# Kernel tuning notes

Measured on AMD Instinct MI355X. Metric: run time of the kernel, lower is better.

Reference implementation:

```python
import jax, jax.numpy as jnp
import numpy as np

DIM = 256
NUM_HEADS = 8
HEAD_DIM = DIM // NUM_HEADS  # 32
SCALE = HEAD_DIM ** (-0.5)


def _conv1x1(x, w, b):
    # x: [B,C,H,W], w: [O,C,1,1], b: [O]
    return jnp.einsum('bchw,oc->bohw', x, w[:, :, 0, 0]) + b[None, :, None, None]


def _dwconv3x3(x, w, b):
    # depthwise conv, groups=C, padding=1 (SAME)
    y = jax.lax.conv_general_dilated(
        x, w, window_strides=(1, 1), padding='SAME',
        feature_group_count=x.shape[1],
        dimension_numbers=('NCHW', 'OIHW', 'NCHW'))
    return y + b[None, :, None, None]


def setup_inputs() -> dict:
    key = jax.random.key(0)
    ks = jax.random.split(key, 9)
    s = 0.05
    return {
        'x': jax.random.normal(ks[0], (4, DIM, 48, 48), jnp.float32),
        'w_qk': jax.random.normal(ks[1], (2 * DIM, DIM, 1, 1), jnp.float32) * s,
        'b_qk': jax.random.normal(ks[2], (2 * DIM,), jnp.float32) * s,
        'w_v': jax.random.normal(ks[3], (DIM, DIM, 1, 1), jnp.float32) * s,
        'b_v': jax.random.normal(ks[4], (DIM,), jnp.float32) * s,
        'w_pe': jax.random.normal(ks[5], (DIM, 1, 3, 3), jnp.float32) * s,
        'b_pe': jax.random.normal(ks[6], (DIM,), jnp.float32) * s,
        'w_proj': jax.random.normal(ks[7], (DIM, DIM, 1, 1), jnp.float32) * s,
        'b_proj': jax.random.normal(ks[8], (DIM,), jnp.float32) * s,
    }


def reference(x, w_qk, b_qk, w_v, b_v, w_pe, b_pe, w_proj, b_proj):
    B, C, H, W = x.shape
    N = H * W
    h, d = NUM_HEADS, HEAD_DIM

    qk = _conv1x1(x, w_qk, b_qk).reshape(B, h, 2 * d, N)
    v4 = _conv1x1(x, w_v, b_v)                # [B,C,H,W]
    pe = _dwconv3x3(v4, w_pe, b_pe)           # [B,C,H,W]
    v = v4.reshape(B, h, d, N)

    q, k = qk[:, :, :d, :], qk[:, :, d:, :]   # [B,h,d,N] each
    attn = jnp.einsum('bhdi,bhdj->bhij', q, k) * SCALE  # [B,h,N,N]
    attn = jax.nn.softmax(attn, axis=-1)
    out = jnp.einsum('bhdj,bhij->bhdi', v, attn)        # [B,h,d,N]
    out = out.reshape(B, C, H, W)

    return _conv1x1(out + pe, w_proj, b_proj)
```

## Files before the change

kernel.cpp:

```cpp
#include <hip/hip_runtime.h>
#include <hip/hip_bf16.h>

#define NPIX 2304
#define HW 48
#define CDIM 256
#define NHEADS 8
#define HD 32
#define SCALE_CONST 0.17677669529663687f
#define LOG2E 1.4426950408889634f

typedef __attribute__((ext_vector_type(8))) short  short8v;
typedef __attribute__((ext_vector_type(4))) short  short4v;
typedef __attribute__((ext_vector_type(4))) float  floatx4;

__device__ inline short f2bf(float f) {
    unsigned u = __builtin_bit_cast(unsigned, f);
    u += 0x7FFFu + ((u >> 16) & 1u);
    return (short)(u >> 16);
}
__device__ inline float bf2f(unsigned short us) {
    return __builtin_bit_cast(float, (unsigned)us << 16);
}
__device__ inline float fexp2(float x) {
    return __builtin_amdgcn_exp2f(x);
}

__global__ __launch_bounds__(256) void prep_kernel(
    const float* __restrict__ x,
    short* __restrict__ XT,
    const float* __restrict__ wqk, const float* __restrict__ wv,
    const float* __restrict__ wp,
    short* __restrict__ wqkb, short* __restrict__ wvb, short* __restrict__ wpb)
{
    const int bx = blockIdx.x;
    const int t = threadIdx.x;
    if (bx >= 576) {
        int tid = (bx - 576) * 256 + t;
        for (int idx = tid; idx < 262144; idx += 16384) {
            if (idx < 131072)       wqkb[idx] = f2bf(wqk[idx]);
            else if (idx < 196608)  wvb[idx - 131072] = f2bf(wv[idx - 131072]);
            else                    wpb[idx - 196608] = f2bf(wp[idx - 196608]);
        }
        return;
    }
    __shared__ float sT[64][65];
    const int nt = bx % 36, ct = (bx / 36) & 3, b = bx / 144;
    const int c0 = ct * 64, n0 = nt * 64;
    const float* sp = x + ((size_t)b * 256 + c0) * NPIX + n0;
    const int cl = t >> 6, n = t & 63;
#pragma unroll
    for (int it = 0; it < 16; ++it) {
        int c = it * 4 + cl;
        sT[n][c] = sp[(size_t)c * NPIX + n];
    }
    __syncthreads();
    const int nr = t >> 2, q = t & 3;
    short out[16];
#pragma unroll
    for (int j = 0; j < 16; ++j) out[j] = f2bf(sT[nr][q * 16 + j]);
    short* dp = XT + ((size_t)b * NPIX + n0 + nr) * 256 + c0 + q * 16;
    *(int4*)dp = *(int4*)out;
    *(int4*)(dp + 8) = *(int4*)(out + 8);
}

#define XROW 528

__device__ inline void stage_xt_tile(const short* __restrict__ src_base,
                                     char* __restrict__ sX, int t)
{
    const short* src = src_base + (size_t)(t >> 3) * 256 + (t & 7) * 32;
    char* dst = sX + (t >> 3) * XROW + (t & 7) * 64;
#pragma unroll
    for (int rr = 0; rr < 2; ++rr) {
        const short* s = src + rr * 32 * 256;
        char* d = dst + rr * 32 * XROW;
        *(int4*)d        = *(const int4*)s;
        *(int4*)(d + 16) = *(const int4*)(s + 8);
        *(int4*)(d + 32) = *(const int4*)(s + 16);
        *(int4*)(d + 48) = *(const int4*)(s + 24);
    }
}

__global__ __launch_bounds__(256) void conv_qkv_mfma(
    const short* __restrict__ Wqk,
    const short* __restrict__ Wv,
    const float* __restrict__ bqk,
    const float* __restrict__ bv,
    const short* __restrict__ XT,
    short* __restrict__ QT,
    short* __restrict__ KT,
    short* __restrict__ VB)
{
    __shared__ __align__(16) char sX[64 * XROW];
    const int n0 = blockIdx.x * 64;
    const int b  = blockIdx.z;
    const int t = threadIdx.x, lane = t & 63, w = t >> 6;
    const int l15 = lane & 15, quad = lane >> 4;

    stage_xt_tile(XT + ((size_t)b * NPIX + n0) * 256, sX, t);
    __syncthreads();

    floatx4 accs[2][4];
#pragma unroll
    for (int g = 0; g < 2; ++g) {
        const int og = blockIdx.y + g * 6;
        const bool isV = (og >= 8);
        const short* Wb = isV ? Wv + (size_t)((og - 8) * 64 + w * 16 + l15) * CDIM
                              : Wqk + (size_t)(og * 64 + w * 16 + l15) * CDIM;
#pragma unroll
        for (int ib = 0; ib < 4; ++ib) accs[g][ib] = (floatx4){0.f, 0.f, 0.f, 0.f};
#pragma unroll
        for (int s = 0; s < 8; ++s) {
            short8v af = *(const short8v*)(Wb + s * 32 + quad * 8);
#pragma unroll
            for (int ib = 0; ib < 4; ++ib) {
                short8v bf = *(const short8v*)(sX + (ib * 16 + l15) * XROW + s * 64 + quad * 16);
                accs[g][ib] = __builtin_amdgcn_mfma_f32_16x16x32_bf16(af, bf, accs[g][ib], 0, 0, 0);
            }
        }
    }

#pragma unroll
    for (int g = 0; g < 2; ++g) {
        const int og = blockIdx.y + g * 6;
        const bool isV = (og >= 8);
        __syncthreads();
        if (!isV) {
            const bool isQ = (w < 2);
            const float scl = isQ ? SCALE_CONST * LOG2E : 1.0f;
            float bvv[4];
#pragma unroll
            for (int r = 0; r < 4; ++r) bvv[r] = bqk[og * 64 + w * 16 + quad * 4 + r];
#pragma unroll
            for (int ib = 0; ib < 4; ++ib) {
                short pb[4];
#pragma unroll
                for (int r = 0; r < 4; ++r) pb[r] = f2bf((accs[g][ib][r] + bvv[r]) * scl);
                *(short4v*)(sX + (ib * 16 + l15) * 136 + (w * 16 + quad * 4) * 2) = *(short4v*)pb;
            }
            __syncthreads();
            const int n = t >> 2, q = t & 3;
            int4 v0 = *(const int4*)(sX + n * 136 + q * 32);
            int4 v1 = *(const int4*)(sX + n * 136 + q * 32 + 16);
            short* dst = ((q < 2) ? QT : KT)
                       + ((size_t)(b * 8 + og) * NPIX + n0 + n) * HD + (q & 1) * 16;
            *(int4*)dst = v0;
            *(int4*)(dst + 8) = v1;
        } else {
            const int o0 = (og - 8) * 64 + w * 16 + quad * 4;
            float bvv[4];
#pragma unroll
            for (int r = 0; r < 4; ++r) bvv[r] = bv[o0 + r];
#pragma unroll
            for (int ib = 0; ib < 4; ++ib) {
                short pb[4];
#pragma unroll
                for (int r = 0; r < 4; ++r) pb[r] = f2bf(accs[g][ib][r] + bvv[r]);
                *(short4v*)(sX + (ib * 16 + l15) * 132 + (w * 16 + quad * 4) * 2) = *(short4v*)pb;
            }
            __syncthreads();
            const int o = t >> 2, q = t & 3;
            short tmp[16];
#pragma unroll
            for (int k = 0; k < 16; ++k)
                tmp[k] = *(const short*)(sX + (q * 16 + k) * 132 + o * 2);
            short* dst = VB + ((size_t)b * 256 + (og - 8) * 64 + o) * NPIX + n0 + q * 16;
            *(int4*)dst = *(int4*)tmp;
            *(int4*)(dst + 8) = *(int4*)(tmp + 8);
        }
    }
}

#define DROW 170

__global__ __launch_bounds__(256) void dwconv3x3_t(
    const short* __restrict__ VB,
    const float* __restrict__ Wp,
    const float* __restrict__ bp,
    short* __restrict__ PEt)
{
    __shared__ short spl[32 * DROW];
    const int n0 = blockIdx.x * 64;
    const int c0 = blockIdx.y * 32;
    const int b  = blockIdx.z;
    const int t  = threadIdx.x;

    for (int ch8 = t; ch8 < 672; ch8 += 256) {
        int ch = ch8 / 21, off = (ch8 % 21) * 8;
        int base = n0 - 52 + off;
        const short* src = VB + ((size_t)b * 256 + c0 + ch) * NPIX;
        short tmp[8];
        if (base >= 0 && base + 8 <= NPIX) {
            *(int4*)tmp = *(const int4*)(src + base);
        } else {
#pragma unroll
            for (int u = 0; u < 8; ++u) {
                int p = base + u;
                tmp[u] = (p >= 0 && p < NPIX) ? src[p] : (short)0;
            }
        }
        *(int4*)&spl[ch * DROW + off] = *(int4*)tmp;
    }
    __syncthreads();

    const int cl = t & 31;
    const int g8 = t >> 5;
    const int c  = c0 + cl;
    float wv[9];
#pragma unroll
    for (int k = 0; k < 9; ++k) wv[k] = Wp[c * 9 + k];
    const float bb = bp[c];

    const int px0  = n0 + g8 * 8;
    const int col0 = px0 % HW;
    const short* sprow = &spl[cl * DROW + 52 + g8 * 8];

#pragma unroll
    for (int u = 0; u < 8; ++u) {
        int colu = col0 + u; if (colu >= HW) colu -= HW;
        const bool okL = (colu != 0), okR = (colu != HW - 1);
        float a = bb;
#pragma unroll
        for (int dy = 0; dy < 3; ++dy) {
            int ci = u + (dy - 1) * HW;
            float m = bf2f((unsigned short)sprow[ci]);
            a += wv[dy * 3 + 1] * m;
            if (okL) a += wv[dy * 3 + 0] * bf2f((unsigned short)sprow[ci - 1]);
            if (okR) a += wv[dy * 3 + 2] * bf2f((unsigned short)sprow[ci + 1]);
        }
        PEt[((size_t)b * NPIX + px0 + u) * 256 + c] = f2bf(a);
    }
}

#define KROW 72
#define VROW 136
#define PROW 136
#define SK0 0
#define SK1 4608
#define SV0 9216
#define SV1 13568
#define SP0 17920
#define FL_SMEM 26624

__global__ __launch_bounds__(256) void flash_attn_mfma(
    const short* __restrict__ QT,
    const short* __restrict__ KT,
    const short* __restrict__ VB,
    const short* __restrict__ PEt,
    short* __restrict__ ST)
{
    __shared__ __align__(16) char smem[FL_SMEM];

    const int i0 = blockIdx.x * 64;
    const int bh = blockIdx.y;
    const int b  = bh >> 3, hh = bh & 7;

    const short* KTp = KT + (size_t)bh * NPIX * HD;
    const short* Vp  = VB + (size_t)(b * 256 + hh * HD) * NPIX;

    const int t    = threadIdx.x;
    const int lane = t & 63;
    const int w    = t >> 6;
    const int l15  = lane & 15;
    const int quad = lane >> 4;

    const short8v qfrag = *(const short8v*)(
        QT + ((size_t)bh * NPIX + i0 + w * 16 + l15) * HD + quad * 8);

    short8v ones;
#pragma unroll
    for (int k = 0; k < 8; ++k) ones[k] = (short)0x3F80;

    char* const sPw = smem + SP0 + w * (16 * PROW);

    floatx4 oacc[2], lacc;
    oacc[0] = (floatx4){0.f, 0.f, 0.f, 0.f};
    oacc[1] = (floatx4){0.f, 0.f, 0.f, 0.f};
    lacc    = (floatx4){0.f, 0.f, 0.f, 0.f};

    const short* ksrc = KTp + (size_t)(t >> 2) * HD + (t & 3) * 8;
    const short* vsrc = Vp + (size_t)(t >> 3) * NPIX + (t & 7) * 8;
    const int koff = (t >> 2) * KROW + (t & 3) * 16;
    const int voff = (t >> 3) * VROW + (t & 7) * 16;

    int4 kst = *(const int4*)ksrc;
    int4 vst = *(const int4*)vsrc;

    for (int it = 0; it < 36; ++it) {
        char* bufK = smem + ((it & 1) ? SK1 : SK0);
        char* bufV = smem + ((it & 1) ? SV1 : SV0);
        *(int2*)(bufK + koff)     = *(int2*)&kst;
        *(int2*)(bufK + koff + 8) = *((int2*)&kst + 1);
        *(int2*)(bufV + voff)     = *(int2*)&vst;
        *(int2*)(bufV + voff + 8) = *((int2*)&vst + 1);
        if (it + 1 < 36) {
            kst = *(const int4*)(ksrc + (size_t)(it + 1) * 64 * HD);
            vst = *(const int4*)(vsrc + (it + 1) * 64);
        }
        __syncthreads();

        floatx4 sacc[4];
#pragma unroll
        for (int jb = 0; jb < 4; ++jb) {
            const char* ka = bufK + (jb * 16 + l15) * KROW + quad * 16;
            short8v af;
            ((int2*)&af)[0] = *(const int2*)ka;
            ((int2*)&af)[1] = *(const int2*)(ka + 8);
            sacc[jb] = __builtin_amdgcn_mfma_f32_16x16x32_bf16(
                af, qfrag, (floatx4){0.f, 0.f, 0.f, 0.f}, 0, 0, 0);
        }

#pragma unroll
        for (int jb = 0; jb < 4; ++jb) {
            unsigned tb[4];
#pragma unroll
            for (int r = 0; r < 4; ++r)
                tb[r] = __builtin_bit_cast(unsigned, fexp2(sacc[jb][r]));
            int2 pw;
            pw.x = (int)__builtin_amdgcn_perm(tb[1], tb[0], 0x07060302u);
            pw.y = (int)__builtin_amdgcn_perm(tb[3], tb[2], 0x07060302u);
            *(int2*)(sPw + l15 * PROW + jb * 32 + quad * 8) = pw;
        }

#pragma unroll
        for (int ks = 0; ks < 2; ++ks) {
            const char* pa = sPw + l15 * PROW + ks * 64 + quad * 16;
            short8v pf;
            ((int2*)&pf)[0] = *(const int2*)pa;
            ((int2*)&pf)[1] = *(const int2*)(pa + 8);
#pragma unroll
            for (int db = 0; db < 2; ++db) {
                const char* va = bufV + (db * 16 + l15) * VROW + ks * 64 + quad * 16;
                short8v vf;
                ((int2*)&vf)[0] = *(const int2*)va;
                ((int2*)&vf)[1] = *(const int2*)(va + 8);
                oacc[db] = __builtin_amdgcn_mfma_f32_16x16x32_bf16(vf, pf, oacc[db], 0, 0, 0);
            }
            lacc = __builtin_amdgcn_mfma_f32_16x16x32_bf16(ones, pf, lacc, 0, 0, 0);
        }
    }

    const float invl = 1.0f / lacc[0];
    const int i = i0 + w * 16 + l15;
    const short* pep = PEt + ((size_t)b * NPIX + i) * 256 + hh * HD;
    short* stp = ST + ((size_t)b * NPIX + i) * 256 + hh * HD;
#pragma unroll
    for (int db = 0; db < 2; ++db) {
        short4v pev = *(const short4v*)(pep + db * 16 + quad * 4);
        short pb[4];
#pragma unroll
        for (int r = 0; r < 4; ++r) {
            float v = oacc[db][r] * invl + bf2f((unsigned short)pev[r]);
            pb[r] = f2bf(v);
        }
        *(short4v*)(stp + db * 16 + quad * 4) = *(short4v*)pb;
    }
}

__global__ __launch_bounds__(256) void conv_proj_mfma(
    const short* __restrict__ Wb,
    const float* __restrict__ bias,
    const short* __restrict__ ST,
    float* __restrict__ out)
{
    __shared__ __align__(16) char sX[64 * XROW];
    const int n0 = blockIdx.x * 64;
    const int og = blockIdx.y;
    const int b  = blockIdx.z;
    const int t = threadIdx.x, lane = t & 63, w = t >> 6;
    const int l15 = lane & 15, quad = lane >> 4;

    stage_xt_tile(ST + ((size_t)b * NPIX + n0) * 256, sX, t);
    __syncthreads();

    const short* Arow = Wb + (size_t)(og * 64 + w * 16 + l15) * CDIM;
    floatx4 acc[4];
#pragma unroll
    for (int ib = 0; ib < 4; ++ib) acc[ib] = (floatx4){0.f, 0.f, 0.f, 0.f};
#pragma unroll
    for (int s = 0; s < 8; ++s) {
        short8v af = *(const short8v*)(Arow + s * 32 + quad * 8);
#pragma unroll
        for (int ib = 0; ib < 4; ++ib) {
            short8v bf = *(const short8v*)(sX + (ib * 16 + l15) * XROW + s * 64 + quad * 16);
            acc[ib] = __builtin_amdgcn_mfma_f32_16x16x32_bf16(af, bf, acc[ib], 0, 0, 0);
        }
    }
    __syncthreads();

    {
        float bvv[4];
#pragma unroll
        for (int r = 0; r < 4; ++r) bvv[r] = bias[og * 64 + w * 16 + quad * 4 + r];
        float* sRep = (float*)sX;
#pragma unroll
        for (int r = 0; r < 4; ++r)
#pragma unroll
            for (int ib = 0; ib < 4; ++ib)
                sRep[(w * 16 + quad * 4 + r) * 68 + ib * 16 + l15] = acc[ib][r] + bvv[r];
    }
    __syncthreads();

    const int o = t >> 2, q = t & 3;
    const float* src = (const float*)sX + o * 68 + q * 16;
    float* dst = out + ((size_t)b * 256 + og * 64 + o) * NPIX + n0 + q * 16;
#pragma unroll
    for (int k = 0; k < 4; ++k)
        *(int4*)(dst + k * 4) = *(const int4*)(src + k * 4);
}

extern "C" void kernel_launch(void* const* d_in, const int* in_sizes, int n_in,
                              void* d_out, int out_size, void* d_ws, size_t ws_size,
                              hipStream_t stream) {
    const float* x      = (const float*)d_in[0];
    const float* w_qk   = (const float*)d_in[1];
    const float* b_qk   = (const float*)d_in[2];
    const float* w_v    = (const float*)d_in[3];
    const float* b_v    = (const float*)d_in[4];
    const float* w_pe   = (const float*)d_in[5];
    const float* b_pe   = (const float*)d_in[6];
    const float* w_proj = (const float*)d_in[7];
    const float* b_proj = (const float*)d_in[8];
    float* out = (float*)d_out;

    char* wsb = (char*)d_ws;
    short* ws_xt  = (short*)wsb;  wsb += (size_t)4 * NPIX * 256 * 2;
    short* ws_qt  = (short*)wsb;  wsb += (size_t)32 * NPIX * HD * 2;
    short* ws_kt  = (short*)wsb;  wsb += (size_t)32 * NPIX * HD * 2;
    short* ws_vb  = (short*)wsb;  wsb += (size_t)4 * 256 * NPIX * 2;
    short* ws_pet = (short*)wsb;  wsb += (size_t)4 * NPIX * 256 * 2;
    short* ws_st  = (short*)wsb;  wsb += (size_t)4 * NPIX * 256 * 2;
    short* ws_wqk = (short*)wsb;  wsb += (size_t)512 * 256 * 2;
    short* ws_wv  = (short*)wsb;  wsb += (size_t)256 * 256 * 2;
    short* ws_wp  = (short*)wsb;  wsb += (size_t)256 * 256 * 2;

    prep_kernel<<<dim3(640), 256, 0, stream>>>(x, ws_xt, w_qk, w_v, w_proj,
                                               ws_wqk, ws_wv, ws_wp);
    conv_qkv_mfma<<<dim3(36, 6, 4), 256, 0, stream>>>(ws_wqk, ws_wv, b_qk, b_v,
                                                      ws_xt, ws_qt, ws_kt, ws_vb);
    dwconv3x3_t<<<dim3(36, 8, 4), 256, 0, stream>>>(ws_vb, w_pe, b_pe, ws_pet);
    flash_attn_mfma<<<dim3(36, 32), 256, 0, stream>>>(ws_qt, ws_kt, ws_vb, ws_pet, ws_st);
    conv_proj_mfma<<<dim3(36, 4, 4), 256, 0, stream>>>(ws_wp, b_proj, ws_st, out);
}
```

Before: 161.0 us.

## Fuse depthwise 3x3 positional conv into output projection kernel

Removes the standalone depthwise-conv kernel and its PE intermediate buffer. The projection kernel now stages V halos for all 256 channels, computes the 3x3 depthwise conv itself, adds the result to the staged attention output tile in shared memory, and then runs the projection GEMM. Each block now covers two output-channel groups, so the grid halves. This saves one launch plus a write and read of the PE tensor. In exchange, every projection block recomputes the dwconv for all channels, which means redundant work across the 2 y-blocks, and the larger shared-memory footprint may lower occupancy.

New measurement: 179.3 us. 1.11x slower.

```diff
diff --git a/kernel.cpp b/kernel.cpp
--- a/kernel.cpp
+++ b/kernel.cpp
@@ -171,67 +171,6 @@
     }
 }
 
-#define DROW 170
-
-__global__ __launch_bounds__(256) void dwconv3x3_t(
-    const short* __restrict__ VB,
-    const float* __restrict__ Wp,
-    const float* __restrict__ bp,
-    short* __restrict__ PEt)
-{
-    __shared__ short spl[32 * DROW];
-    const int n0 = blockIdx.x * 64;
-    const int c0 = blockIdx.y * 32;
-    const int b  = blockIdx.z;
-    const int t  = threadIdx.x;
-
-    for (int ch8 = t; ch8 < 672; ch8 += 256) {
-        int ch = ch8 / 21, off = (ch8 % 21) * 8;
-        int base = n0 - 52 + off;
-        const short* src = VB + ((size_t)b * 256 + c0 + ch) * NPIX;
-        short tmp[8];
-        if (base >= 0 && base + 8 <= NPIX) {
-            *(int4*)tmp = *(const int4*)(src + base);
-        } else {
-#pragma unroll
-            for (int u = 0; u < 8; ++u) {
-                int p = base + u;
-                tmp[u] = (p >= 0 && p < NPIX) ? src[p] : (short)0;
-            }
-        }
-        *(int4*)&spl[ch * DROW + off] = *(int4*)tmp;
-    }
-    __syncthreads();
-
-    const int cl = t & 31;
-    const int g8 = t >> 5;
-    const int c  = c0 + cl;
-    float wv[9];
-#pragma unroll
-    for (int k = 0; k < 9; ++k) wv[k] = Wp[c * 9 + k];
-    const float bb = bp[c];
-
-    const int px0  = n0 + g8 * 8;
-    const int col0 = px0 % HW;
-    const short* sprow = &spl[cl * DROW + 52 + g8 * 8];
-
-#pragma unroll
-    for (int u = 0; u < 8; ++u) {
-        int colu = col0 + u; if (colu >= HW) colu -= HW;
-        const bool okL = (colu != 0), okR = (colu != HW - 1);
-        float a = bb;
-#pragma unroll
-        for (int dy = 0; dy < 3; ++dy) {
-            int ci = u + (dy - 1) * HW;
-            float m = bf2f((unsigned short)sprow[ci]);
-            a += wv[dy * 3 + 1] * m;
-            if (okL) a += wv[dy * 3 + 0] * bf2f((unsigned short)sprow[ci - 1]);
-            if (okR) a += wv[dy * 3 + 2] * bf2f((unsigned short)sprow[ci + 1]);
-        }
-        PEt[((size_t)b * NPIX + px0 + u) * 256 + c] = f2bf(a);
-    }
-}
-
 #define KROW 72
 #define VROW 136
 #define PROW 136
@@ -246,7 +185,6 @@
     const short* __restrict__ QT,
     const short* __restrict__ KT,
     const short* __restrict__ VB,
-    const short* __restrict__ PEt,
     short* __restrict__ ST)
 {
     __shared__ __align__(16) char smem[FL_SMEM];
@@ -342,71 +280,138 @@
 
     const float invl = 1.0f / lacc[0];
     const int i = i0 + w * 16 + l15;
-    const short* pep = PEt + ((size_t)b * NPIX + i) * 256 + hh * HD;
     short* stp = ST + ((size_t)b * NPIX + i) * 256 + hh * HD;
 #pragma unroll
     for (int db = 0; db < 2; ++db) {
-        short4v pev = *(const short4v*)(pep + db * 16 + quad * 4);
         short pb[4];
 #pragma unroll
-        for (int r = 0; r < 4; ++r) {
-            float v = oacc[db][r] * invl + bf2f((unsigned short)pev[r]);
-            pb[r] = f2bf(v);
-        }
+        for (int r = 0; r < 4; ++r)
+            pb[r] = f2bf(oacc[db][r] * invl);
         *(short4v*)(stp + db * 16 + quad * 4) = *(short4v*)pb;
     }
 }
 
-__global__ __launch_bounds__(256) void conv_proj_mfma(
+#define DROW 170
+#define PD_SMEM (64 * XROW + 64 * DROW * 2)
+
+__global__ __launch_bounds__(256) void conv_proj_dw_mfma(
     const short* __restrict__ Wb,
     const float* __restrict__ bias,
+    const float* __restrict__ Wp,
+    const float* __restrict__ bp,
     const short* __restrict__ ST,
+    const short* __restrict__ VB,
     float* __restrict__ out)
 {
-    __shared__ __align__(16) char sX[64 * XROW];
-    const int n0 = blockIdx.x * 64;
-    const int og = blockIdx.y;
-    const int b  = blockIdx.z;
+    __shared__ __align__(16) char sX[PD_SMEM];
+    short* const sHalo = (short*)(sX + 64 * XROW);
+
+    const int n0  = blockIdx.x * 64;
+    const int ogp = blockIdx.y;
+    const int b   = blockIdx.z;
     const int t = threadIdx.x, lane = t & 63, w = t >> 6;
     const int l15 = lane & 15, quad = lane >> 4;
 
     stage_xt_tile(ST + ((size_t)b * NPIX + n0) * 256, sX, t);
+
+    auto stage_halo = [&](int cc) {
+        for (int ch8 = t; ch8 < 1344; ch8 += 256) {
+            int ch = ch8 / 21, off = (ch8 % 21) * 8;
+            int base = n0 - 52 + off;
+            const short* src = VB + ((size_t)b * 256 + cc * 64 + ch) * NPIX;
+            short tmp[8];
+            if (base >= 0 && base + 8 <= NPIX) {
+                *(int4*)tmp = *(const int4*)(src + base);
+            } else {
+#pragma unroll
+                for (int u = 0; u < 8; ++u) {
+                    int p = base + u;
+                    tmp[u] = (p >= 0 && p < NPIX) ? src[p] : (short)0;
+                }
+            }
+            *(int4*)&sHalo[ch * DROW + off] = *(int4*)tmp;
+        }
+    };
+
+    stage_halo(0);
     __syncthreads();
 
-    const short* Arow = Wb + (size_t)(og * 64 + w * 16 + l15) * CDIM;
-    floatx4 acc[4];
-#pragma unroll
-    for (int ib = 0; ib < 4; ++ib) acc[ib] = (floatx4){0.f, 0.f, 0.f, 0.f};
-#pragma unroll
-    for (int s = 0; s < 8; ++s) {
-        short8v af = *(const short8v*)(Arow + s * 32 + quad * 8);
-#pragma unroll
-        for (int ib = 0; ib < 4; ++ib) {
-            short8v bf = *(const short8v*)(sX + (ib * 16 + l15) * XROW + s * 64 + quad * 16);
-            acc[ib] = __builtin_amdgcn_mfma_f32_16x16x32_bf16(af, bf, acc[ib], 0, 0, 0);
-        }
-    }
-    __syncthreads();
-
-    {
-        float bvv[4];
-#pragma unroll
-        for (int r = 0; r < 4; ++r) bvv[r] = bias[og * 64 + w * 16 + quad * 4 + r];
-        float* sRep = (float*)sX;
-#pragma unroll
-        for (int r = 0; r < 4; ++r)
-#pragma unroll
-            for (int ib = 0; ib < 4; ++ib)
-                sRep[(w * 16 + quad * 4 + r) * 68 + ib * 16 + l15] = acc[ib][r] + bvv[r];
-    }
-    __syncthreads();
-
-    const int o = t >> 2, q = t & 3;
-    const float* src = (const float*)sX + o * 68 + q * 16;
-    float* dst = out + ((size_t)b * 256 + og * 64 + o) * NPIX + n0 + q * 16;
-#pragma unroll
-    for (int k = 0; k < 4; ++k)
-        *(int4*)(dst + k * 4) = *(const int4*)(src + k * 4);
+    const int cl = t & 63;
+    const int pg = t >> 6;
+    const int px0  = n0 + pg * 16;
+    const int col0 = px0 % HW;
+
+    for (int cc = 0; cc < 4; ++cc) {
+        const int c = cc * 64 + cl;
+        float wv[9];
+#pragma unroll
+        for (int k = 0; k < 9; ++k) wv[k] = Wp[c * 9 + k];
+        const float bb = bp[c];
+        const short* sprow = &sHalo[cl * DROW + 52 + pg * 16];
+
+#pragma unroll
+        for (int u = 0; u < 16; ++u) {
+            int colu = col0 + u;
+            const bool okL = (colu != 0), okR = (colu != HW - 1);
+            float a = bb;
+#pragma unroll
+            for (int dy = 0; dy < 3; ++dy) {
+                int ci = u + (dy - 1) * HW;
+                a += wv[dy * 3 + 1] * bf2f((unsigned short)sprow[ci]);
+                if (okL) a += wv[dy * 3 + 0] * bf2f((unsigned short)sprow[ci - 1]);
+                if (okR) a += wv[dy * 3 + 2] * bf2f((unsigned short)sprow[ci + 1]);
+            }
+            short* cell = (short*)(sX + (pg * 16 + u) * XROW + c * 2);
+            *cell = f2bf(bf2f((unsigned short)*cell) + a);
+        }
+        __syncthreads();
+        if (cc < 3) {
+            stage_halo(cc + 1);
+            __syncthreads();
+        }
+    }
+
+    floatx4 accs[2][4];
+#pragma unroll
+    for (int g = 0; g < 2; ++g) {
+        const int og = ogp * 2 + g;
+        const short* Arow = Wb + (size_t)(og * 64 + w * 16 + l15) * CDIM;
+#pragma unroll
+        for (int ib = 0; ib < 4; ++ib) accs[g][ib] = (floatx4){0.f, 0.f, 0.f, 0.f};
+#pragma unroll
+        for (int s = 0; s < 8; ++s) {
+            short8v af = *(const short8v*)(Arow + s * 32 + quad * 8);
+#pragma unroll
+            for (int ib = 0; ib < 4; ++ib) {
+                short8v bf = *(const short8v*)(sX + (ib * 16 + l15) * XROW + s * 64 + quad * 16);
+                accs[g][ib] = __builtin_amdgcn_mfma_f32_16x16x32_bf16(af, bf, accs[g][ib], 0, 0, 0);
+            }
+        }
+    }
+
+    float* sRep = (float*)sHalo;
+#pragma unroll
+    for (int g = 0; g < 2; ++g) {
+        const int og = ogp * 2 + g;
+        __syncthreads();
+        {
+            float bvv[4];
+#pragma unroll
+            for (int r = 0; r < 4; ++r) bvv[r] = bias[og * 64 + w * 16 + quad * 4 + r];
+#pragma unroll
+            for (int r = 0; r < 4; ++r)
+#pragma unroll
+                for (int ib = 0; ib < 4; ++ib)
+                    sRep[(w * 16 + quad * 4 + r) * 68 + ib * 16 + l15] = accs[g][ib][r] + bvv[r];
+        }
+        __syncthreads();
+        const int o = t >> 2, q = t & 3;
+        const float* src = sRep + o * 68 + q * 16;
+        float* dst = out + ((size_t)b * 256 + og * 64 + o) * NPIX + n0 + q * 16;
+#pragma unroll
+        for (int k = 0; k < 4; ++k)
+            *(int4*)(dst + k * 4) = *(const int4*)(src + k * 4);
+    }
 }
 
 extern "C" void kernel_launch(void* const* d_in, const int* in_sizes, int n_in,
@@ -428,7 +433,6 @@
     short* ws_qt  = (short*)wsb;  wsb += (size_t)32 * NPIX * HD * 2;
     short* ws_kt  = (short*)wsb;  wsb += (size_t)32 * NPIX * HD * 2;
     short* ws_vb  = (short*)wsb;  wsb += (size_t)4 * 256 * NPIX * 2;
-    short* ws_pet = (short*)wsb;  wsb += (size_t)4 * NPIX * 256 * 2;
     short* ws_st  = (short*)wsb;  wsb += (size_t)4 * NPIX * 256 * 2;
     short* ws_wqk = (short*)wsb;  wsb += (size_t)512 * 256 * 2;
     short* ws_wv  = (short*)wsb;  wsb += (size_t)256 * 256 * 2;
@@ -438,7 +442,7 @@
                                                ws_wqk, ws_wv, ws_wp);
     conv_qkv_mfma<<<dim3(36, 6, 4), 256, 0, stream>>>(ws_wqk, ws_wv, b_qk, b_v,
                                                       ws_xt, ws_qt, ws_kt, ws_vb);
-    dwconv3x3_t<<<dim3(36, 8, 4), 256, 0, stream>>>(ws_vb, w_pe, b_pe, ws_pet);
-    flash_attn_mfma<<<dim3(36, 32), 256, 0, stream>>>(ws_qt, ws_kt, ws_vb, ws_pet, ws_st);
-    conv_proj_mfma<<<dim3(36, 4, 4), 256, 0, stream>>>(ws_wp, b_proj, ws_st, out);
-}
+    flash_attn_mfma<<<dim3(36, 32), 256, 0, stream>>>(ws_qt, ws_kt, ws_vb, ws_st);
+    conv_proj_dw_mfma<<<dim3(36, 2, 4), 256, 0, stream>>>(ws_wp, b_proj, w_pe, b_pe,
+                                                          ws_st, ws_vb, out);
+}
```
